# Kernel optimization log

Hardware: AMD Instinct MI355X
Metric: run time of the kernel (lower is better)

Reference implementation:

```python
import jax, jax.numpy as jnp
import numpy as np

D_MODEL = 1024
N_HEADS = 16
D_HEAD = D_MODEL // N_HEADS
WINDOW = 256
SCALE = D_HEAD ** -0.5


def setup_inputs() -> dict:
    key = jax.random.key(0)
    k1, k2, k3, k4, k5 = jax.random.split(key, 5)
    B, S = 2, 2048
    x = jax.random.normal(k1, (B, S, D_MODEL), dtype=jnp.float32)
    s = 0.02
    Wqkv = jax.random.normal(k2, (D_MODEL, 3 * D_MODEL), dtype=jnp.float32) * s
    bqkv = jnp.zeros((3 * D_MODEL,), dtype=jnp.float32)
    Wout = jax.random.normal(k3, (D_MODEL, D_MODEL), dtype=jnp.float32) * s
    bout = jnp.zeros((D_MODEL,), dtype=jnp.float32)
    return {"x": x, "Wqkv": Wqkv, "bqkv": bqkv, "Wout": Wout, "bout": bout}


def reference(x, Wqkv, bqkv, Wout, bout):
    B, S, D = x.shape
    qkv = x @ Wqkv + bqkv                       # (B, S, 3D)
    q, k, v = jnp.split(qkv, 3, axis=-1)
    # (B, H, S, d)
    q = q.reshape(B, S, N_HEADS, D_HEAD).transpose(0, 2, 1, 3)
    k = k.reshape(B, S, N_HEADS, D_HEAD).transpose(0, 2, 1, 3)
    v = v.reshape(B, S, N_HEADS, D_HEAD).transpose(0, 2, 1, 3)
    scores = jnp.einsum('bhqd,bhkd->bhqk', q, k) * SCALE
    # windowed causal mask: allow j <= i and j >= i - WINDOW (inclusive),
    # matching torch code where mask[i, :i-window_size] = 0 for i >= window_size
    i = jnp.arange(S)[:, None]
    j = jnp.arange(S)[None, :]
    allowed = (j <= i) & (j >= i - WINDOW)      # (S, S)
    scores = jnp.where(allowed[None, None], scores, -jnp.inf)
    attn = jax.nn.softmax(scores, axis=-1)      # dropout=0 / eval mode
    out = jnp.einsum('bhqk,bhkd->bhqd', attn, v)
    out = out.transpose(0, 2, 1, 3).reshape(B, S, D)
    return out @ Wout + bout
```

## Files before the change

### kernel.cpp

```cpp
#include <hip/hip_runtime.h>
#include <stdint.h>


typedef __attribute__((ext_vector_type(8))) short bf16x8;
typedef __attribute__((ext_vector_type(4))) float f32x4;
typedef __attribute__((ext_vector_type(4))) unsigned int u32x4;
typedef __attribute__((ext_vector_type(4))) unsigned short u16x4;

#define DEV static __device__ __forceinline__

#define SC2 0.18033688011112042f

DEV unsigned short f2bf(float f) {
  unsigned int u = __builtin_bit_cast(unsigned int, f);
  u += 0x7fffu + ((u >> 16) & 1u);
  return (unsigned short)(u >> 16);
}

DEV void gload_lds16(const void* g, void* l) {
  __builtin_amdgcn_global_load_lds((const __attribute__((address_space(1))) void*)g,
                                   (__attribute__((address_space(3))) void*)l,
                                   16, 0, 0);
}

__global__ __launch_bounds__(256) void k_prep(const float* __restrict__ x,
                                              const float* __restrict__ Wqkv,
                                              const float* __restrict__ Wout,
                                              const float* __restrict__ bqkv,
                                              unsigned short* __restrict__ xb,
                                              unsigned short* __restrict__ wqT,
                                              unsigned short* __restrict__ woT,
                                              float* __restrict__ bqkv_s) {
  __shared__ float t[32][33];
  const int bid = blockIdx.x, tid = threadIdx.x;
  if (bid < 4096) {
    int i = bid * 256 + tid;
    f32x4 v = ((const f32x4*)x)[i];
    u16x4 o;
    o[0] = f2bf(v[0]); o[1] = f2bf(v[1]); o[2] = f2bf(v[2]); o[3] = f2bf(v[3]);
    ((u16x4*)xb)[i] = o;
    return;
  }
  if (bid >= 8192) {
    int i = (bid - 8192) * 256 + tid;
    if (i < 3072) bqkv_s[i] = bqkv[i] * (i < 1024 ? SC2 : 1.0f);
    return;
  }
  const float* in;
  unsigned short* out;
  int N, K, n0, k0;
  float wscale = 1.0f;
  if (bid < 7168) {
    int tt = bid - 4096;
    in = Wqkv; out = wqT; N = 3072; K = 1024;
    n0 = (tt % 96) * 32; k0 = (tt / 96) * 32;
    if (n0 < 1024) wscale = SC2;
  } else {
    int tt = bid - 7168;
    in = Wout; out = woT; N = 1024; K = 1024;
    n0 = (tt % 32) * 32; k0 = (tt / 32) * 32;
  }
  const int tx = tid & 31, ty = tid >> 5;
#pragma unroll
  for (int i = 0; i < 4; ++i)
    t[ty + i * 8][tx] = in[(size_t)(k0 + ty + i * 8) * N + n0 + tx];
  __syncthreads();
#pragma unroll
  for (int i = 0; i < 4; ++i)
    out[(size_t)(n0 + ty + i * 8) * K + k0 + tx] = f2bf(t[tx][ty + i * 8] * wscale);
}

template <int BN, bool F32OUT, bool FUSE_VT>
__global__ __launch_bounds__(256) void k_gemm(const unsigned short* __restrict__ A,
                                              const unsigned short* __restrict__ Bt,
                                              const float* __restrict__ bias,
                                              void* __restrict__ Cout,
                                              unsigned short* __restrict__ vT,
                                              int M, int N, int K) {
  constexpr int NI = BN / 32;
  constexpr int NCH = 16 + BN / 8;
  __shared__ unsigned short As[2][128 * 64];
  __shared__ unsigned short Bs[2][BN * 64];
  const int tid = threadIdx.x;
  const int lane = tid & 63, wid = tid >> 6;
  const int wr = wid >> 1, wc = wid & 1;
  const int g = lane >> 4, li = lane & 15;
  const int m0 = blockIdx.y * 128, n0 = blockIdx.x * BN;

  f32x4 acc[4][NI] = {};

  const int nkt = K >> 6;
  const int r8 = lane >> 3, sp = lane & 7;

  auto stage = [&](int bufi, int kt) {
#pragma unroll
    for (int c = wid; c < NCH; c += 4) {
      if (c < 16) {
        int row = c * 8 + r8;
        int sl = sp ^ (row & 7);
        gload_lds16(A + (size_t)(m0 + row) * K + kt * 64 + sl * 8,
                    &As[bufi][c * 512]);
      } else {
        int cc = c - 16;
        int row = cc * 8 + r8;
        int sl = sp ^ (row & 7);
        gload_lds16(Bt + (size_t)(n0 + row) * K + kt * 64 + sl * 8,
                    &Bs[bufi][cc * 512]);
      }
    }
  };

  stage(0, 0);
  for (int kt = 0; kt < nkt; ++kt) {
    __syncthreads();
    if (kt + 1 < nkt) stage((kt + 1) & 1, kt + 1);
    const unsigned short* Ac = As[kt & 1];
    const unsigned short* Bc = Bs[kt & 1];
#pragma unroll
    for (int h = 0; h < 2; ++h) {
      bf16x8 af[4], bfr[NI];
#pragma unroll
      for (int mi = 0; mi < 4; ++mi) {
        const int r = wr * 64 + mi * 16 + li;
        const int slot = (g + h * 4) ^ (r & 7);
        af[mi] = *(const bf16x8*)&Ac[r * 64 + slot * 8];
      }
#pragma unroll
      for (int ni = 0; ni < NI; ++ni) {
        const int r = wc * (BN / 2) + ni * 16 + li;
        const int slot = (g + h * 4) ^ (r & 7);
        bfr[ni] = *(const bf16x8*)&Bc[r * 64 + slot * 8];
      }
#pragma unroll
      for (int mi = 0; mi < 4; ++mi)
#pragma unroll
        for (int ni = 0; ni < NI; ++ni)
          acc[mi][ni] = __builtin_amdgcn_mfma_f32_16x16x32_bf16(af[mi], bfr[ni],
                                                                acc[mi][ni], 0, 0, 0);
    }
  }

  float bv[NI];
#pragma unroll
  for (int ni = 0; ni < NI; ++ni) bv[ni] = bias[n0 + wc * (BN / 2) + ni * 16 + li];
#pragma unroll
  for (int mi = 0; mi < 4; ++mi) {
#pragma unroll
    for (int ni = 0; ni < NI; ++ni) {
      const int col = n0 + wc * (BN / 2) + ni * 16 + li;
      const int row0 = m0 + wr * 64 + mi * 16 + g * 4;
      float v0 = acc[mi][ni][0] + bv[ni];
      float v1 = acc[mi][ni][1] + bv[ni];
      float v2 = acc[mi][ni][2] + bv[ni];
      float v3 = acc[mi][ni][3] + bv[ni];
      if (F32OUT) {
        float* C = (float*)Cout;
        C[(size_t)(row0 + 0) * N + col] = v0;
        C[(size_t)(row0 + 1) * N + col] = v1;
        C[(size_t)(row0 + 2) * N + col] = v2;
        C[(size_t)(row0 + 3) * N + col] = v3;
      } else {
        unsigned short* C = (unsigned short*)Cout;
        C[(size_t)(row0 + 0) * N + col] = f2bf(v0);
        C[(size_t)(row0 + 1) * N + col] = f2bf(v1);
        C[(size_t)(row0 + 2) * N + col] = f2bf(v2);
        C[(size_t)(row0 + 3) * N + col] = f2bf(v3);
      }
      if (FUSE_VT && col >= 2048) {
        const int b = row0 >> 11;
        const int s = row0 & 2047;
        u16x4 vv;
        vv[0] = f2bf(v0); vv[1] = f2bf(v1); vv[2] = f2bf(v2); vv[3] = f2bf(v3);
        *(u16x4*)&vT[(size_t)(b * 1024 + col - 2048) * 2048 + s] = vv;
      }
    }
  }
}

__global__ __launch_bounds__(256) void k_attn3(const unsigned short* __restrict__ qkv,
                                               const unsigned short* __restrict__ vT,
                                               unsigned short* __restrict__ attn) {
  __shared__ unsigned short Ks[2][64 * 64];
  __shared__ unsigned short Vs[2][64 * 64];
  __shared__ unsigned short Ps[64 * 88];
  const int tid = threadIdx.x, lane = tid & 63, wid = tid >> 6;
  const int g = lane >> 4, li = lane & 15;
  const int bh = blockIdx.y, b = bh >> 4, h = bh & 15;
  const int q0 = blockIdx.x * 64;
  const size_t rs = 3072;
  const unsigned short* qb = qkv + (size_t)b * 2048 * rs + h * 64;
  const unsigned short* kb = qb + 1024;
  const unsigned short* vb = vT + (size_t)bh * 64 * 2048;

  const int qrow = wid * 16 + li;
  const bf16x8 qf0 = *(const bf16x8*)(qb + (size_t)(q0 + qrow) * rs + (g << 3));
  const bf16x8 qf1 = *(const bf16x8*)(qb + (size_t)(q0 + qrow) * rs + 32 + (g << 3));

  const int tf = (blockIdx.x >= 4) ? 0 : (4 - (int)blockIdx.x);

  auto stage = [&](int bufi, int t) {
    const int j0 = q0 - 256 + t * 64;
    const int sl = (lane & 7) ^ ((lane >> 3) & 7);
#pragma unroll
    for (int j = 0; j < 2; ++j) {
      const int chunk = wid * 2 + j;
      const int row = chunk * 8 + (lane >> 3);
      gload_lds16(kb + (size_t)(j0 + row) * rs + sl * 8, &Ks[bufi][chunk * 512]);
      gload_lds16(vb + (size_t)row * 2048 + j0 + sl * 8, &Vs[bufi][chunk * 512]);
    }
  };

  f32x4 o[4] = {};
  float l_part[4] = {0.f, 0.f, 0.f, 0.f};

  stage(0, tf);
  int cur = 0;
  for (int t = tf; t < 5; ++t) {
    if (t + 1 < 5) {
      stage(cur ^ 1, t + 1);
      asm volatile("s_waitcnt vmcnt(4)" ::: "memory");
    } else {
      asm volatile("s_waitcnt vmcnt(0)" ::: "memory");
    }
    __builtin_amdgcn_sched_barrier(0);
    __builtin_amdgcn_s_barrier();
    __builtin_amdgcn_sched_barrier(0);

    const unsigned short* Kc = Ks[cur];
    const unsigned short* Vc = Vs[cur];

    f32x4 s[4];
#pragma unroll
    for (int ni = 0; ni < 4; ++ni) {
      const int kr = ni * 16 + li;
      const int sw = (kr & 7);
      bf16x8 kf0 = *(const bf16x8*)&Kc[kr * 64 + ((g ^ sw) << 3)];
      bf16x8 kf1 = *(const bf16x8*)&Kc[kr * 64 + (((4 + g) ^ sw) << 3)];
      f32x4 z = {};
      z = __builtin_amdgcn_mfma_f32_16x16x32_bf16(qf0, kf0, z, 0, 0, 0);
      z = __builtin_amdgcn_mfma_f32_16x16x32_bf16(qf1, kf1, z, 0, 0, 0);
      s[ni] = z;
    }
    const int rt = wid * 16 + g * 4;
#pragma unroll
    for (int ni = 0; ni < 4; ++ni) {
      int ct = ni * 16 + li;
#pragma unroll
      for (int reg = 0; reg < 4; ++reg) {
        float sv = s[ni][reg];
        if (t == 4 && ct > rt + reg) sv = -3e30f;
        if (t == 0 && ct < rt + reg) sv = -3e30f;
        s[ni][reg] = sv;
      }
    }
#pragma unroll
    for (int reg = 0; reg < 4; ++reg) {
      float ps = 0.f;
#pragma unroll
      for (int ni = 0; ni < 4; ++ni) {
        float p = __builtin_exp2f(s[ni][reg] - 16.0f);
        ps += p;
        Ps[(wid * 16 + g * 4 + reg) * 88 + ni * 16 + li] = f2bf(p);
      }
      l_part[reg] += ps;
    }
    asm volatile("s_waitcnt lgkmcnt(0)" ::: "memory");
    __builtin_amdgcn_sched_barrier(0);
    const bf16x8 pf0 = *(const bf16x8*)&Ps[(wid * 16 + li) * 88 + (g << 3)];
    const bf16x8 pf1 = *(const bf16x8*)&Ps[(wid * 16 + li) * 88 + 32 + (g << 3)];
#pragma unroll
    for (int ni = 0; ni < 4; ++ni) {
      const int dr = ni * 16 + li;
      const int sw = (dr & 7);
      bf16x8 vf0 = *(const bf16x8*)&Vc[dr * 64 + ((g ^ sw) << 3)];
      bf16x8 vf1 = *(const bf16x8*)&Vc[dr * 64 + (((4 + g) ^ sw) << 3)];
      o[ni] = __builtin_amdgcn_mfma_f32_16x16x32_bf16(pf0, vf0, o[ni], 0, 0, 0);
      o[ni] = __builtin_amdgcn_mfma_f32_16x16x32_bf16(pf1, vf1, o[ni], 0, 0, 0);
    }
    __builtin_amdgcn_sched_barrier(0);
    __builtin_amdgcn_s_barrier();
    cur ^= 1;
  }

  float inv[4];
#pragma unroll
  for (int reg = 0; reg < 4; ++reg) {
    float L = l_part[reg];
    L += __shfl_xor(L, 1, 64);
    L += __shfl_xor(L, 2, 64);
    L += __shfl_xor(L, 4, 64);
    L += __shfl_xor(L, 8, 64);
    inv[reg] = 1.f / L;
  }
#pragma unroll
  for (int ni = 0; ni < 4; ++ni) {
#pragma unroll
    for (int reg = 0; reg < 4; ++reg) {
      size_t row = (size_t)b * 2048 + q0 + wid * 16 + g * 4 + reg;
      attn[row * 1024 + h * 64 + ni * 16 + li] = f2bf(o[ni][reg] * inv[reg]);
    }
  }
}

extern "C" void kernel_launch(void* const* d_in, const int* in_sizes, int n_in,
                              void* d_out, int out_size, void* d_ws, size_t ws_size,
                              hipStream_t stream) {
  const float* x    = (const float*)d_in[0];
  const float* Wqkv = (const float*)d_in[1];
  const float* bqkv = (const float*)d_in[2];
  const float* Wout = (const float*)d_in[3];
  const float* bout = (const float*)d_in[4];
  float* out = (float*)d_out;

  uint8_t* ws = (uint8_t*)d_ws;
  unsigned short* xb    = (unsigned short*)(ws);
  unsigned short* wqT   = (unsigned short*)(ws +  8388608);
  unsigned short* woT   = (unsigned short*)(ws + 14680064);
  unsigned short* qkvb  = (unsigned short*)(ws + 16777216);
  unsigned short* attnb = (unsigned short*)(ws + 41943040);
  unsigned short* vTb   = (unsigned short*)(ws + 50331648);
  float*          bqs   = (float*)(ws + 58720256);

  k_prep<<<8204, 256, 0, stream>>>(x, Wqkv, Wout, bqkv, xb, wqT, woT, bqs);
  k_gemm<192, false, true><<<dim3(3072 / 192, 4096 / 128), 256, 0, stream>>>(
      xb, wqT, bqs, qkvb, vTb, 4096, 3072, 1024);
  k_attn3<<<dim3(2048 / 64, 32), 256, 0, stream>>>(qkvb, vTb, attnb);
  k_gemm<64, true, false><<<dim3(1024 / 64, 4096 / 128), 256, 0, stream>>>(
      attnb, woT, bout, out, nullptr, 4096, 1024, 1024);
}
```

Measured before the change: 89.70 us.

## Enlarge GEMM M-tile to 256 rows with 512 threads and dynamic LDS

Both GEMMs now use 256-row M tiles computed by 8 waves per block, with shared memory moved to a dynamically sized buffer (up to 112 KB). Each B tile is reused across twice as many rows, which halves the B-operand global traffic per output and doubles the work per block. The cost is fewer blocks in flight (the QKV GEMM drops to 256 blocks), far higher LDS use per block that may limit occupancy, and possibly larger tail effects. Warp row indexing (wr = wid>>1 now spans 0..3) appears to extend coverage to 256 rows, but the epilogue code is not visible.

```diff
diff --git a/kernel.cpp b/kernel.cpp
--- a/kernel.cpp
+++ b/kernel.cpp
@@ -71,41 +71,45 @@
 }
 
 template <int BN, bool F32OUT, bool FUSE_VT>
-__global__ __launch_bounds__(256) void k_gemm(const unsigned short* __restrict__ A,
-                                              const unsigned short* __restrict__ Bt,
-                                              const float* __restrict__ bias,
-                                              void* __restrict__ Cout,
-                                              unsigned short* __restrict__ vT,
-                                              int M, int N, int K) {
+__global__ __launch_bounds__(512) void k_gemmbig(const unsigned short* __restrict__ A,
+                                                 const unsigned short* __restrict__ Bt,
+                                                 const float* __restrict__ bias,
+                                                 void* __restrict__ Cout,
+                                                 unsigned short* __restrict__ vT,
+                                                 int M, int N, int K) {
   constexpr int NI = BN / 32;
-  constexpr int NCH = 16 + BN / 8;
-  __shared__ unsigned short As[2][128 * 64];
-  __shared__ unsigned short Bs[2][BN * 64];
+  constexpr int ACH = 32;
+  constexpr int NCH = ACH + BN / 8;
+  constexpr int ASZ = 256 * 64;
+  constexpr int BSZ = BN * 64;
+  extern __shared__ unsigned short lds[];
   const int tid = threadIdx.x;
   const int lane = tid & 63, wid = tid >> 6;
   const int wr = wid >> 1, wc = wid & 1;
   const int g = lane >> 4, li = lane & 15;
-  const int m0 = blockIdx.y * 128, n0 = blockIdx.x * BN;
+  const int m0 = blockIdx.y * 256, n0 = blockIdx.x * BN;
 
   f32x4 acc[4][NI] = {};
-
   const int nkt = K >> 6;
   const int r8 = lane >> 3, sp = lane & 7;
 
+  auto Abuf = [&](int i) { return lds + i * ASZ; };
+  auto Bbuf = [&](int i) { return lds + 2 * ASZ + i * BSZ; };
+
   auto stage = [&](int bufi, int kt) {
 #pragma unroll
-    for (int c = wid; c < NCH; c += 4) {
-      if (c < 16) {
+    for (int c = wid; c < NCH; c += 8) {
+      if (c < ACH) {
         int row = c * 8 + r8;
         int sl = sp ^ (row & 7);
         gload_lds16(A + (size_t)(m0 + row) * K + kt * 64 + sl * 8,
-                    &As[bufi][c * 512]);
+                    Abuf(bufi) + c * 512);
       } else {
-        int cc = c - 16;
+        int cc = c - ACH;
         int row = cc * 8 + r8;
         int sl = sp ^ (row & 7);
         gload_lds16(Bt + (size_t)(n0 + row) * K + kt * 64 + sl * 8,
-                    &Bs[bufi][cc * 512]);
+                    Bbuf(bufi) + cc * 512);
       }
     }
   };
@@ -114,8 +118,8 @@
   for (int kt = 0; kt < nkt; ++kt) {
     __syncthreads();
     if (kt + 1 < nkt) stage((kt + 1) & 1, kt + 1);
-    const unsigned short* Ac = As[kt & 1];
-    const unsigned short* Bc = Bs[kt & 1];
+    const unsigned short* Ac = Abuf(kt & 1);
+    const unsigned short* Bc = Bbuf(kt & 1);
 #pragma unroll
     for (int h = 0; h < 2; ++h) {
       bf16x8 af[4], bfr[NI];
@@ -321,10 +325,15 @@
   unsigned short* vTb   = (unsigned short*)(ws + 50331648);
   float*          bqs   = (float*)(ws + 58720256);
 
+  hipFuncSetAttribute((const void*)k_gemmbig<192, false, true>,
+                      hipFuncAttributeMaxDynamicSharedMemorySize, 114688);
+  hipFuncSetAttribute((const void*)k_gemmbig<64, true, false>,
+                      hipFuncAttributeMaxDynamicSharedMemorySize, 81920);
+
   k_prep<<<8204, 256, 0, stream>>>(x, Wqkv, Wout, bqkv, xb, wqT, woT, bqs);
-  k_gemm<192, false, true><<<dim3(3072 / 192, 4096 / 128), 256, 0, stream>>>(
+  k_gemmbig<192, false, true><<<dim3(3072 / 192, 4096 / 256), 512, 114688, stream>>>(
       xb, wqT, bqs, qkvb, vTb, 4096, 3072, 1024);
   k_attn3<<<dim3(2048 / 64, 32), 256, 0, stream>>>(qkvb, vTb, attnb);
-  k_gemm<64, true, false><<<dim3(1024 / 64, 4096 / 128), 256, 0, stream>>>(
+  k_gemmbig<64, true, false><<<dim3(1024 / 64, 4096 / 256), 512, 81920, stream>>>(
       attnb, woT, bout, out, nullptr, 4096, 1024, 1024);
 }
```

Measured after the change: 85.73 us. 1.05x faster.
